# Kernel optimization log

Hardware: AMD Instinct MI355X
Metric: run time of the kernel (lower is better)

Reference implementation:

```python
import jax, jax.numpy as jnp
import numpy as np

N_QUBITS = 14
N_LAYERS = 4
N_CLASSES = 10
BATCH = 1024


def apply_1q(state, gate, wire):
    """Apply a 2x2 gate ([2,2] shared or [B,2,2] batched) to `wire` of state [B,2,...,2]."""
    s = jnp.moveaxis(state, wire + 1, -1)
    shp = s.shape
    s = s.reshape(shp[0], -1, 2)
    if gate.ndim == 3:
        s = jnp.einsum('bij,bkj->bki', gate, s)
    else:
        s = jnp.einsum('ij,bkj->bki', gate, s)
    return jnp.moveaxis(s.reshape(shp), -1, wire + 1)


def apply_cnot(state, c, t):
    s = jnp.moveaxis(state, (c + 1, t + 1), (-2, -1))
    s = jnp.stack([s[..., 0, :], s[..., 1, ::-1]], axis=-2)
    return jnp.moveaxis(s, (-2, -1), (c + 1, t + 1))


def simulate(x, q_params):
    """Batched statevector sim of: RY(x_i) embed -> BasicEntanglerLayers(RX + CNOT ring) -> <Z_i>."""
    B, n = x.shape
    state = jnp.zeros((B,) + (2,) * n, jnp.complex64)
    state = state.at[(slice(None),) + (0,) * n].set(1.0)

    # RY(x_i) on each wire (angles batched per sample)
    c, s = jnp.cos(0.5 * x), jnp.sin(0.5 * x)
    for w in range(n):
        g = jnp.stack([jnp.stack([c[:, w], -s[:, w]], -1),
                       jnp.stack([s[:, w], c[:, w]], -1)], -2).astype(jnp.complex64)  # [B,2,2]
        state = apply_1q(state, g, w)

    # BasicEntanglerLayers: per layer RX(weights[l,i]) on every wire, then CNOT ring
    cw, sw = jnp.cos(0.5 * q_params), jnp.sin(0.5 * q_params)
    n_layers = q_params.shape[0]
    for l in range(n_layers):
        for w in range(n):
            cc = cw[l, w].astype(jnp.complex64)
            isw = (-1j) * sw[l, w].astype(jnp.complex64)
            g = jnp.stack([jnp.stack([cc, isw]), jnp.stack([isw, cc])])  # [2,2] RX
            state = apply_1q(state, g, w)
        if n == 2:
            state = apply_cnot(state, 0, 1)
        else:
            for w in range(n):
                state = apply_cnot(state, w, (w + 1) % n)

    # <Z_i> = P(bit_i=0) - P(bit_i=1)
    p = jnp.abs(state) ** 2  # [B,2,...,2] real
    axes_all = tuple(range(1, n + 1))
    z = []
    for w in range(n):
        pw = jnp.sum(p, axis=tuple(a for a in axes_all if a != w + 1))  # [B,2]
        z.append(pw[:, 0] - pw[:, 1])
    return jnp.stack(z, -1).astype(jnp.float32)  # [B, n]


def setup_inputs() -> dict:
    key = jax.random.key(0)
    k1, k2, k3, k4 = jax.random.split(key, 4)
    x = jax.random.normal(k1, (BATCH, N_QUBITS), dtype=jnp.float32)
    q_params = 0.01 * jax.random.normal(k2, (N_LAYERS, N_QUBITS), dtype=jnp.float32)
    fc_w = jax.random.normal(k3, (N_CLASSES, N_QUBITS), dtype=jnp.float32) / np.sqrt(N_QUBITS)
    fc_b = jax.random.normal(k4, (N_CLASSES,), dtype=jnp.float32) * 0.01
    return {"x": x, "q_params": q_params, "fc_w": fc_w, "fc_b": fc_b}


def reference(x, q_params, fc_w, fc_b):
    q_out = simulate(x, q_params)            # [B, n_qubits]
    logits = q_out @ fc_w.T + fc_b           # [B, n_classes]
    return logits
```

## Files before the change

kernel.cpp:

```cpp
#include <hip/hip_runtime.h>
#include <hip/hip_fp16.h>
#include <math.h>


#define NQ 14
#define NSTATE (1 << NQ)
#define NLAYERS 4
#define NCLASSES 10
#define BLOCK 512
#define PADN (NSTATE + (NSTATE >> 5))

template<int LO, int M, int STEP, bool IS_RX, bool INIT, int PRE_CTRL, int POST_CTRL, bool CHAIN, bool FINAL>
__device__ __forceinline__ void run_pass(__half2* __restrict__ st,
                                         const __half2* __restrict__ cw,
                                         const __half2* __restrict__ sw,
                                         float* __restrict__ zloc)
{
  constexpr int KN  = 1 << M;
  constexpr int NCH = NSTATE >> M;
  __half2 c[M], s[M];
#pragma unroll
  for (int j = 0; j < M; ++j) { c[j] = cw[j]; s[j] = sw[j]; }

  for (int chunk = threadIdx.x; chunk < NCH; chunk += BLOCK) {
    const int low   = chunk & ((1 << LO) - 1);
    const int high  = chunk >> LO;
    const int base  = low | (high << (LO + M));
    const int pbase = base + (base >> 5);
    __half2 a[KN];
    if constexpr (INIT) {
#pragma unroll
      for (int k = 0; k < KN; ++k) a[k] = __floats2half2_rn(0.f, 0.f);
      if (chunk == 0) a[0] = __floats2half2_rn(1.f, 0.f);
    } else {
#pragma unroll
      for (int k = 0; k < KN; ++k) a[k] = st[pbase + k * STEP];
    }
    if constexpr (PRE_CTRL >= 0) {
      if ((base >> PRE_CTRL) & 1) {
#pragma unroll
        for (int k = 0; k < KN; k += 2) { __half2 t = a[k]; a[k] = a[k + 1]; a[k + 1] = t; }
      }
    }
#pragma unroll
    for (int j = 0; j < M; ++j) {
#pragma unroll
      for (int k = 0; k < KN; ++k) {
        if ((k & (1 << j)) == 0) {
          const int k1 = k | (1 << j);
          const __half2 a0 = a[k], a1 = a[k1];
          if constexpr (IS_RX) {
            a[k]  = __hfma2(s[j], __lowhigh2highlow(a1), __hmul2(c[j], a0));
            a[k1] = __hfma2(s[j], __lowhigh2highlow(a0), __hmul2(c[j], a1));
          } else {
            a[k]  = __hsub2(__hmul2(c[j], a0), __hmul2(s[j], a1));
            a[k1] = __hfma2(s[j], a0, __hmul2(c[j], a1));
          }
        }
      }
    }
    if constexpr (POST_CTRL >= 0) {
      if ((base >> POST_CTRL) & 1) {
#pragma unroll
        for (int k = 0; k < KN; k += 2) { __half2 t = a[k]; a[k] = a[k + 1]; a[k + 1] = t; }
      }
    }
    if constexpr (CHAIN) {
#pragma unroll
      for (int j = 0; j < M - 1; ++j) {
#pragma unroll
        for (int k = 0; k < KN; ++k) {
          if ((k & (1 << j)) != 0 && (k & (1 << (j + 1))) == 0) {
            const int k2 = k | (1 << (j + 1));
            __half2 t = a[k]; a[k] = a[k2]; a[k2] = t;
          }
        }
      }
    }
    if constexpr (FINAL) {
      float ssum = 0.f, sb0 = 0.f, sb1 = 0.f, sb2 = 0.f, sb3 = 0.f;
#pragma unroll
      for (int k = 0; k < KN; ++k) {
        const float2 v = __half22float2(a[k]);
        const float p = fmaf(v.x, v.x, v.y * v.y);
        ssum += p;
        if (k & 1) sb0 += p;
        if (k & 2) sb1 += p;
        if (k & 4) sb2 += p;
        if (k & 8) sb3 += p;
      }
      zloc[10] += ssum - 2.f * sb0;
      zloc[11] += ssum - 2.f * sb1;
      zloc[12] += ssum - 2.f * sb2;
      zloc[13] += ssum - 2.f * sb3;
      const float z0 = ssum - 2.f * sb3;
      zloc[0] += (base & 1) ? -z0 : z0;
#pragma unroll
      for (int w = 1; w < 10; ++w) zloc[w] += ((base >> w) & 1) ? -ssum : ssum;
    } else {
#pragma unroll
      for (int k = 0; k < KN; ++k) st[pbase + k * STEP] = a[k];
    }
  }
}

__global__ __launch_bounds__(BLOCK) void qsim_kernel(
    const float* __restrict__ x, const float* __restrict__ qp,
    const float* __restrict__ fcw, const float* __restrict__ fcb,
    float* __restrict__ out)
{
  extern __shared__ unsigned char smem[];
  __half2* st  = (__half2*)smem;
  __half2* ryc = st + PADN;
  __half2* rys = ryc + NQ;
  __half2* rxc = rys + NQ;
  __half2* rxs = rxc + NLAYERS * NQ;
  float*   zbuf  = (float*)(rxs + NLAYERS * NQ);
  float*   zpart = zbuf + NQ;

  const int b   = blockIdx.x;
  const int tid = threadIdx.x;

  if (tid < NQ) {
    float sv, cv;
    sincosf(0.5f * x[b * NQ + tid], &sv, &cv);
    ryc[tid] = __floats2half2_rn(cv, cv);
    rys[tid] = __floats2half2_rn(sv, sv);
  } else if (tid >= 64 && tid < 64 + NLAYERS * NQ) {
    const int k = tid - 64;
    float sv, cv;
    sincosf(0.5f * qp[k], &sv, &cv);
    rxc[k] = __floats2half2_rn(cv, cv);
    rxs[k] = __floats2half2_rn(sv, -sv);
  }
  __syncthreads();

  run_pass<0, 5, 1,    false, true,  -1, -1, false, false>(st, ryc,      rys,      nullptr); __syncthreads();
  run_pass<5, 5, 33,   false, false, -1, -1, false, false>(st, ryc + 5,  rys + 5,  nullptr); __syncthreads();
  run_pass<10, 4, 1056,false, false, -1, -1, false, false>(st, ryc + 10, rys + 10, nullptr); __syncthreads();

  float zloc[NQ];
#pragma unroll
  for (int w = 0; w < NQ; ++w) zloc[w] = 0.f;

#pragma unroll
  for (int l = 0; l < NLAYERS; ++l) {
    const __half2* lc = rxc + l * NQ;
    const __half2* ls = rxs + l * NQ;
    if (l == 0) run_pass<0, 5, 1, true, false, -1, -1, true, false>(st, lc, ls, nullptr);
    else        run_pass<0, 5, 1, true, false, 13, -1, true, false>(st, lc, ls, nullptr);
    __syncthreads();
    run_pass<5, 5, 33, true, false, -1, 4, true, false>(st, lc + 5, ls + 5, nullptr);
    __syncthreads();
    if (l < NLAYERS - 1) {
      run_pass<10, 4, 1056, true, false, -1, 9, true, false>(st, lc + 10, ls + 10, nullptr);
      __syncthreads();
    } else {
      run_pass<10, 4, 1056, true, false, -1, 9, true, true>(st, lc + 10, ls + 10, zloc);
    }
  }

#pragma unroll
  for (int w = 0; w < NQ; ++w) {
#pragma unroll
    for (int off = 32; off > 0; off >>= 1)
      zloc[w] += __shfl_down(zloc[w], off, 64);
  }
  const int wave = tid >> 6, lane = tid & 63;
  if (lane == 0) {
#pragma unroll
    for (int w = 0; w < NQ; ++w) zpart[wave * NQ + w] = zloc[w];
  }
  __syncthreads();
  if (tid < NQ) {
    float acc = 0.f;
#pragma unroll
    for (int v = 0; v < BLOCK / 64; ++v) acc += zpart[v * NQ + tid];
    zbuf[tid] = acc;
  }
  __syncthreads();

  if (tid < NCLASSES) {
    float acc = fcb[tid];
#pragma unroll
    for (int w = 0; w < NQ; ++w) acc = fmaf(zbuf[w], fcw[tid * NQ + w], acc);
    out[b * NCLASSES + tid] = acc;
  }
}

extern "C" void kernel_launch(void* const* d_in, const int* in_sizes, int n_in,
                              void* d_out, int out_size, void* d_ws, size_t ws_size,
                              hipStream_t stream) {
  const float* x   = (const float*)d_in[0];
  const float* qp  = (const float*)d_in[1];
  const float* fcw = (const float*)d_in[2];
  const float* fcb = (const float*)d_in[3];
  float* out = (float*)d_out;
  const int B = in_sizes[0] / NQ;

  const size_t shmem = (size_t)PADN * sizeof(__half2)
                     + (size_t)(2 * NQ + 2 * NLAYERS * NQ) * sizeof(__half2)
                     + (size_t)(NQ + (BLOCK / 64) * NQ) * sizeof(float);
  (void)hipFuncSetAttribute((const void*)qsim_kernel,
                            hipFuncAttributeMaxDynamicSharedMemorySize, (int)shmem);
  qsim_kernel<<<B, BLOCK, shmem, stream>>>(x, qp, fcw, fcb, out);
}
```

Measured before the change: 145.2 us.

## Rewrite statevector sim as MFMA matrix products with fused RX+CNOT unitaries

Replaces the per-thread half2 butterfly passes with 32x32 and 16x16 complex unitaries, built per layer from RX angles with the CNOT permutations folded in, and applied via f16 MFMA instructions on split real/imaginary planes in LDS with XOR swizzling. The RY embedding plus the first RX block is computed analytically as a product state instead of through passes. This aims to move the gate arithmetic onto matrix cores and cut the number of passes. In exchange it adds per-pass matrix construction, extra barriers, and a larger LDS footprint (about 67KB) that limits blocks per CU.

Measured after the change: 146.1 us. No clear change (+0.6%).

```diff
diff --git a/kernel.cpp b/kernel.cpp
--- a/kernel.cpp
+++ b/kernel.cpp
@@ -4,162 +4,303 @@
 
 
 #define NQ 14
-#define NSTATE (1 << NQ)
 #define NLAYERS 4
 #define NCLASSES 10
 #define BLOCK 512
-#define PADN (NSTATE + (NSTATE >> 5))
-
-template<int LO, int M, int STEP, bool IS_RX, bool INIT, int PRE_CTRL, int POST_CTRL, bool CHAIN, bool FINAL>
-__device__ __forceinline__ void run_pass(__half2* __restrict__ st,
-                                         const __half2* __restrict__ cw,
-                                         const __half2* __restrict__ sw,
-                                         float* __restrict__ zloc)
-{
-  constexpr int KN  = 1 << M;
-  constexpr int NCH = NSTATE >> M;
-  __half2 c[M], s[M];
-#pragma unroll
-  for (int j = 0; j < M; ++j) { c[j] = cw[j]; s[j] = sw[j]; }
-
-  for (int chunk = threadIdx.x; chunk < NCH; chunk += BLOCK) {
-    const int low   = chunk & ((1 << LO) - 1);
-    const int high  = chunk >> LO;
-    const int base  = low | (high << (LO + M));
-    const int pbase = base + (base >> 5);
-    __half2 a[KN];
-    if constexpr (INIT) {
-#pragma unroll
-      for (int k = 0; k < KN; ++k) a[k] = __floats2half2_rn(0.f, 0.f);
-      if (chunk == 0) a[0] = __floats2half2_rn(1.f, 0.f);
+
+typedef _Float16 f16;
+typedef _Float16 f16x8 __attribute__((ext_vector_type(8)));
+typedef _Float16 f16x4 __attribute__((ext_vector_type(4)));
+typedef float f32x4 __attribute__((ext_vector_type(4)));
+typedef unsigned int u32;
+typedef u32 u32x4 __attribute__((ext_vector_type(4)));
+
+__device__ __forceinline__ f32x4 mf(f16x8 a, f16x8 b, f32x4 c) {
+  return __builtin_amdgcn_mfma_f32_16x16x32_f16(a, b, c, 0, 0, 0);
+}
+
+__device__ __forceinline__ int finv5(int n) {
+  n ^= ((n >> 3) & 1) << 4;
+  n ^= ((n >> 2) & 1) << 3;
+  n ^= ((n >> 1) & 1) << 2;
+  n ^= (n & 1) << 1;
+  return n;
+}
+__device__ __forceinline__ int finv3(int n) {
+  n ^= ((n >> 2) & 1) << 3;
+  n ^= ((n >> 1) & 1) << 2;
+  n ^= (n & 1) << 1;
+  return n;
+}
+
+__device__ __forceinline__ void splitB(f16x8 b, int s, f16x8& br, f16x8& bi) {
+  u32x4 u = __builtin_bit_cast(u32x4, b);
+  const u32 m0 = s ? 0xFFFF0000u : 0x0000FFFFu;
+  const u32 m1 = s ? 0x0000FFFFu : 0xFFFF0000u;
+  u32x4 r;
+  r[0] = u[0] & m0; r[1] = u[1] & m1; r[2] = u[2] & m1; r[3] = u[3] & m0;
+  u32x4 ii;
+  ii[0] = u[0] ^ r[0]; ii[1] = u[1] ^ r[1]; ii[2] = u[2] ^ r[2]; ii[3] = u[3] ^ r[3];
+  br = __builtin_bit_cast(f16x8, r);
+  bi = __builtin_bit_cast(f16x8, ii);
+}
+
+__device__ __forceinline__ void build32(f16* Bc, const float* qc, const float* qs,
+                                        int base, int tid) {
+  const float c0 = qc[base], c1 = qc[base+1], c2 = qc[base+2], c3 = qc[base+3], c4 = qc[base+4];
+  const float s0 = qs[base], s1 = qs[base+1], s2 = qs[base+2], s3 = qs[base+3], s4 = qs[base+4];
+#pragma unroll
+  for (int e = tid; e < 1024; e += BLOCK) {
+    const int n = e >> 5, k = e & 31;
+    const int d = finv5(n) ^ k;
+    float mag = ((d & 1) ? s0 : c0) * ((d & 2) ? s1 : c1);
+    mag *= ((d & 4) ? s2 : c2) * ((d & 8) ? s3 : c3);
+    mag *= ((d & 16) ? s4 : c4);
+    const int t = __popc(d) & 3;
+    Bc[n * 32 + k] = (f16)((t == 1 || t == 2) ? -mag : mag);
+  }
+}
+
+__device__ __forceinline__ void buildC(f16* Bc, const float* qc, const float* qs,
+                                       int base, int tid) {
+  const float c0 = qc[base], c1 = qc[base+1], c2 = qc[base+2], c3 = qc[base+3];
+  const float s0 = qs[base], s1 = qs[base+1], s2 = qs[base+2], s3 = qs[base+3];
+  if (tid < 512) {
+    const int n = tid >> 5, k = tid & 31;
+    float v = 0.f;
+    if (k < 16) {
+      const int d = finv3(n) ^ k;
+      float mag = ((d & 1) ? s0 : c0) * ((d & 2) ? s1 : c1);
+      mag *= ((d & 4) ? s2 : c2) * ((d & 8) ? s3 : c3);
+      const int t = __popc(d) & 3;
+      v = (t == 1 || t == 2) ? -mag : mag;
+    }
+    Bc[n * 32 + k] = (f16)v;
+  }
+}
+
+template<bool CTRL>
+__device__ __forceinline__ void pass32(f16* __restrict__ reP, f16* __restrict__ imP,
+                                       const f16* __restrict__ Bc, int tid) {
+  const int lane = tid & 63, wave = tid >> 6;
+  const int q = lane >> 4, cc = lane & 15;
+  int n0 = cc, n1 = cc | 16;
+  if (CTRL && wave >= 4) { n0 ^= 31; n1 ^= 31; }
+  const int pq = (0x6 >> q) & 1;
+  f16x8 br0, bi0, br1, bi1;
+  {
+    const f16x8 b0 = *(const f16x8*)(Bc + n0 * 32 + 8 * q);
+    const f16x8 b1 = *(const f16x8*)(Bc + n1 * 32 + 8 * q);
+    splitB(b0, ((n0 >> 4) ^ pq) & 1, br0, bi0);
+    splitB(b1, ((n1 >> 4) ^ pq) & 1, br1, bi1);
+  }
+  f16x4 outR[8], outI[8];
+#pragma unroll
+  for (int i = 0; i < 4; ++i) {
+    const int mt = wave * 4 + i;
+    const int pA = ((mt * 16 + cc) * 32 + 8 * q) ^ ((mt & 7) << 3);
+    const f16x8 Ar = *(const f16x8*)(reP + pA);
+    const f16x8 Ai = *(const f16x8*)(imP + pA);
+    const f16x8 nAi = -Ai;
+#pragma unroll
+    for (int nt = 0; nt < 2; ++nt) {
+      const f16x8 br = nt ? br1 : br0;
+      const f16x8 bi = nt ? bi1 : bi0;
+      f32x4 aR = {0.f, 0.f, 0.f, 0.f}, aI = {0.f, 0.f, 0.f, 0.f};
+      aR = mf(Ar, br, aR); aR = mf(nAi, bi, aR);
+      aI = mf(Ar, bi, aI); aI = mf(Ai, br, aI);
+      outR[i * 2 + nt] = __builtin_convertvector(aR, f16x4);
+      outI[i * 2 + nt] = __builtin_convertvector(aI, f16x4);
+    }
+  }
+  __syncthreads();
+#pragma unroll
+  for (int i = 0; i < 4; ++i) {
+#pragma unroll
+    for (int nt = 0; nt < 2; ++nt) {
+      const int n5 = nt * 16 + cc;
+      const int rr = (wave * 4 + i) * 16 + 4 * q;
+      const int pS = (rr | (n5 << 9)) ^ ((n5 & 7) << 3);
+      *(f16x4*)(reP + pS) = outR[i * 2 + nt];
+      *(f16x4*)(imP + pS) = outI[i * 2 + nt];
+    }
+  }
+}
+
+template<bool FINAL>
+__device__ __forceinline__ void passC(f16* __restrict__ reP, f16* __restrict__ imP,
+                                      const f16* __restrict__ Bc, int tid,
+                                      float* __restrict__ zloc) {
+  const int lane = tid & 63, wave = tid >> 6;
+  const int q = lane >> 4, cc = lane & 15;
+  int n0 = cc;
+  if (wave >= 4) n0 ^= 15;
+  const int pq = (0x6 >> q) & 1;
+  f16x8 br, bi;
+  {
+    const f16x8 b = *(const f16x8*)(Bc + n0 * 32 + 8 * q);
+    splitB(b, ((n0 >> 3) ^ pq) & 1, br, bi);
+  }
+  f16x4 outR[8], outI[8];
+#pragma unroll
+  for (int i = 0; i < 8; ++i) {
+    const int mt = wave * 8 + i;
+    const int pA = ((mt * 16 + cc) * 16 + 8 * (q & 1)) ^ (((mt >> 1) & 7) << 3);
+    const f16x8 Ar = *(const f16x8*)(reP + pA);
+    const f16x8 Ai = *(const f16x8*)(imP + pA);
+    const f16x8 nAi = -Ai;
+    f32x4 aR = {0.f, 0.f, 0.f, 0.f}, aI = {0.f, 0.f, 0.f, 0.f};
+    aR = mf(Ar, br, aR); aR = mf(nAi, bi, aR);
+    aI = mf(Ar, bi, aI); aI = mf(Ai, br, aI);
+    if constexpr (FINAL) {
+      float p0 = aR[0]*aR[0] + aI[0]*aI[0];
+      float p1 = aR[1]*aR[1] + aI[1]*aI[1];
+      float p2 = aR[2]*aR[2] + aI[2]*aI[2];
+      float p3 = aR[3]*aR[3] + aI[3]*aI[3];
+      if (cc & 8) { float t = p0; p0 = p1; p1 = t; t = p2; p2 = p3; p3 = t; }
+      const float ps = p0 + p1 + p2 + p3;
+      zloc[0] += (p0 - p1) + (p2 - p3);
+      zloc[1] += (p0 + p1) - (p2 + p3);
+      zloc[2] += (q & 1) ? -ps : ps;
+      zloc[3] += (q & 2) ? -ps : ps;
+#pragma unroll
+      for (int w = 0; w < 6; ++w) zloc[4 + w] += ((mt >> w) & 1) ? -ps : ps;
+#pragma unroll
+      for (int w = 0; w < 4; ++w) zloc[10 + w] += ((cc >> w) & 1) ? -ps : ps;
     } else {
-#pragma unroll
-      for (int k = 0; k < KN; ++k) a[k] = st[pbase + k * STEP];
-    }
-    if constexpr (PRE_CTRL >= 0) {
-      if ((base >> PRE_CTRL) & 1) {
-#pragma unroll
-        for (int k = 0; k < KN; k += 2) { __half2 t = a[k]; a[k] = a[k + 1]; a[k + 1] = t; }
+      if (cc & 8) {
+        f32x4 tR = aR, tI = aI;
+        aR[0] = tR[1]; aR[1] = tR[0]; aR[2] = tR[3]; aR[3] = tR[2];
+        aI[0] = tI[1]; aI[1] = tI[0]; aI[2] = tI[3]; aI[3] = tI[2];
       }
-    }
-#pragma unroll
-    for (int j = 0; j < M; ++j) {
-#pragma unroll
-      for (int k = 0; k < KN; ++k) {
-        if ((k & (1 << j)) == 0) {
-          const int k1 = k | (1 << j);
-          const __half2 a0 = a[k], a1 = a[k1];
-          if constexpr (IS_RX) {
-            a[k]  = __hfma2(s[j], __lowhigh2highlow(a1), __hmul2(c[j], a0));
-            a[k1] = __hfma2(s[j], __lowhigh2highlow(a0), __hmul2(c[j], a1));
-          } else {
-            a[k]  = __hsub2(__hmul2(c[j], a0), __hmul2(s[j], a1));
-            a[k1] = __hfma2(s[j], a0, __hmul2(c[j], a1));
-          }
-        }
-      }
-    }
-    if constexpr (POST_CTRL >= 0) {
-      if ((base >> POST_CTRL) & 1) {
-#pragma unroll
-        for (int k = 0; k < KN; k += 2) { __half2 t = a[k]; a[k] = a[k + 1]; a[k + 1] = t; }
-      }
-    }
-    if constexpr (CHAIN) {
-#pragma unroll
-      for (int j = 0; j < M - 1; ++j) {
-#pragma unroll
-        for (int k = 0; k < KN; ++k) {
-          if ((k & (1 << j)) != 0 && (k & (1 << (j + 1))) == 0) {
-            const int k2 = k | (1 << (j + 1));
-            __half2 t = a[k]; a[k] = a[k2]; a[k2] = t;
-          }
-        }
-      }
-    }
-    if constexpr (FINAL) {
-      float ssum = 0.f, sb0 = 0.f, sb1 = 0.f, sb2 = 0.f, sb3 = 0.f;
-#pragma unroll
-      for (int k = 0; k < KN; ++k) {
-        const float2 v = __half22float2(a[k]);
-        const float p = fmaf(v.x, v.x, v.y * v.y);
-        ssum += p;
-        if (k & 1) sb0 += p;
-        if (k & 2) sb1 += p;
-        if (k & 4) sb2 += p;
-        if (k & 8) sb3 += p;
-      }
-      zloc[10] += ssum - 2.f * sb0;
-      zloc[11] += ssum - 2.f * sb1;
-      zloc[12] += ssum - 2.f * sb2;
-      zloc[13] += ssum - 2.f * sb3;
-      const float z0 = ssum - 2.f * sb3;
-      zloc[0] += (base & 1) ? -z0 : z0;
-#pragma unroll
-      for (int w = 1; w < 10; ++w) zloc[w] += ((base >> w) & 1) ? -ssum : ssum;
-    } else {
-#pragma unroll
-      for (int k = 0; k < KN; ++k) st[pbase + k * STEP] = a[k];
-    }
-  }
-}
-
-__global__ __launch_bounds__(BLOCK) void qsim_kernel(
+      outR[i] = __builtin_convertvector(aR, f16x4);
+      outI[i] = __builtin_convertvector(aI, f16x4);
+    }
+  }
+  if constexpr (!FINAL) {
+    __syncthreads();
+#pragma unroll
+    for (int i = 0; i < 8; ++i) {
+      const int rr = (wave * 8 + i) * 16 + 4 * q;
+      const int nI = rr | (cc << 10);
+      const int pS = nI ^ ((((rr >> 9) | ((cc & 3) << 1)) & 7) << 3);
+      *(f16x4*)(reP + pS) = outR[i];
+      *(f16x4*)(imP + pS) = outI[i];
+    }
+  }
+}
+
+__global__ __launch_bounds__(BLOCK, 4) void qsim_kernel(
     const float* __restrict__ x, const float* __restrict__ qp,
     const float* __restrict__ fcw, const float* __restrict__ fcb,
-    float* __restrict__ out)
-{
+    float* __restrict__ out) {
   extern __shared__ unsigned char smem[];
-  __half2* st  = (__half2*)smem;
-  __half2* ryc = st + PADN;
-  __half2* rys = ryc + NQ;
-  __half2* rxc = rys + NQ;
-  __half2* rxs = rxc + NLAYERS * NQ;
-  float*   zbuf  = (float*)(rxs + NLAYERS * NQ);
-  float*   zpart = zbuf + NQ;
-
-  const int b   = blockIdx.x;
+  f16* reP = (f16*)smem;
+  f16* imP = reP + 16384;
+  unsigned char* scr = (unsigned char*)(imP + 16384);
+  f16* Bc = (f16*)scr;
+  float* qc = (float*)(scr + 2048);
+  float* qs = qc + 56;
+  float* xc = qs + 56;
+  float* xs = xc + 14;
+
+  const int b = blockIdx.x;
   const int tid = threadIdx.x;
 
   if (tid < NQ) {
-    float sv, cv;
-    sincosf(0.5f * x[b * NQ + tid], &sv, &cv);
-    ryc[tid] = __floats2half2_rn(cv, cv);
-    rys[tid] = __floats2half2_rn(sv, sv);
+    float sv, cv; sincosf(0.5f * x[b * NQ + tid], &sv, &cv);
+    xc[tid] = cv; xs[tid] = sv;
   } else if (tid >= 64 && tid < 64 + NLAYERS * NQ) {
     const int k = tid - 64;
-    float sv, cv;
-    sincosf(0.5f * qp[k], &sv, &cv);
-    rxc[k] = __floats2half2_rn(cv, cv);
-    rxs[k] = __floats2half2_rn(sv, -sv);
-  }
-  __syncthreads();
-
-  run_pass<0, 5, 1,    false, true,  -1, -1, false, false>(st, ryc,      rys,      nullptr); __syncthreads();
-  run_pass<5, 5, 33,   false, false, -1, -1, false, false>(st, ryc + 5,  rys + 5,  nullptr); __syncthreads();
-  run_pass<10, 4, 1056,false, false, -1, -1, false, false>(st, ryc + 10, rys + 10, nullptr); __syncthreads();
+    float sv, cv; sincosf(0.5f * qp[k], &sv, &cv);
+    qc[k] = cv; qs[k] = sv;
+  }
+  __syncthreads();
+
+  float* Flo  = (float*)scr;
+  float* psi  = Flo + 32;
+  float* PsiR = psi + 32;
+  float* PsiI = PsiR + 32;
+  if (tid < 32) {
+    float f = 1.f;
+#pragma unroll
+    for (int j = 0; j < 5; ++j) f *= ((tid >> j) & 1) ? xs[5 + j] : xc[5 + j];
+    Flo[tid] = f;
+  } else if (tid < 64) {
+    const int k = tid - 32;
+    float f = 1.f;
+#pragma unroll
+    for (int j = 0; j < 5; ++j) f *= ((k >> j) & 1) ? xs[j] : xc[j];
+    psi[k] = f;
+  }
+  __syncthreads();
+  if (tid < 32) {
+    const float c0 = qc[0], c1 = qc[1], c2 = qc[2], c3 = qc[3], c4 = qc[4];
+    const float s0 = qs[0], s1 = qs[1], s2 = qs[2], s3 = qs[3], s4 = qs[4];
+    const int a = finv5(tid);
+    float ar = 0.f, ai = 0.f;
+    for (int k = 0; k < 32; ++k) {
+      const int d = a ^ k;
+      float mag = ((d & 1) ? s0 : c0) * ((d & 2) ? s1 : c1);
+      mag *= ((d & 4) ? s2 : c2) * ((d & 8) ? s3 : c3);
+      mag *= ((d & 16) ? s4 : c4);
+      mag *= psi[k];
+      const int t = __popc(d) & 3;
+      if (t == 0) ar += mag; else if (t == 1) ai -= mag;
+      else if (t == 2) ar -= mag; else ai += mag;
+    }
+    PsiR[tid] = ar; PsiI[tid] = ai;
+  }
+  __syncthreads();
+  {
+    float fhi = 1.f;
+#pragma unroll
+    for (int j = 0; j < 4; ++j) fhi *= ((tid >> j) & 1) ? xs[10 + j] : xc[10 + j];
+    const float cr = fhi * PsiR[tid >> 4], ci = fhi * PsiI[tid >> 4];
+    const int pconst = ((tid >> 4) & 7) << 3;
+#pragma unroll
+    for (int kb = 0; kb < 4; ++kb) {
+      f16x8 hr, hi;
+#pragma unroll
+      for (int j = 0; j < 8; ++j) {
+        const float F = Flo[8 * kb + j];
+        hr[j] = (f16)(F * cr);
+        hi[j] = (f16)(F * ci);
+      }
+      const int pb = (tid * 32 + 8 * kb) ^ pconst;
+      *(f16x8*)(reP + pb) = hr;
+      *(f16x8*)(imP + pb) = hi;
+    }
+  }
+  __syncthreads();
+
+  build32(Bc, qc, qs, 0 * NQ + 5, tid);  __syncthreads();
+  pass32<true>(reP, imP, Bc, tid);       __syncthreads();
+  buildC(Bc, qc, qs, 0 * NQ + 10, tid);  __syncthreads();
+  passC<false>(reP, imP, Bc, tid, nullptr); __syncthreads();
+#pragma unroll
+  for (int l = 1; l < 3; ++l) {
+    build32(Bc, qc, qs, l * NQ + 0, tid);  __syncthreads();
+    pass32<false>(reP, imP, Bc, tid);      __syncthreads();
+    build32(Bc, qc, qs, l * NQ + 5, tid);  __syncthreads();
+    pass32<true>(reP, imP, Bc, tid);       __syncthreads();
+    buildC(Bc, qc, qs, l * NQ + 10, tid);  __syncthreads();
+    passC<false>(reP, imP, Bc, tid, nullptr); __syncthreads();
+  }
+  build32(Bc, qc, qs, 3 * NQ + 0, tid);  __syncthreads();
+  pass32<false>(reP, imP, Bc, tid);      __syncthreads();
+  build32(Bc, qc, qs, 3 * NQ + 5, tid);  __syncthreads();
+  pass32<true>(reP, imP, Bc, tid);       __syncthreads();
+  buildC(Bc, qc, qs, 3 * NQ + 10, tid);  __syncthreads();
 
   float zloc[NQ];
 #pragma unroll
   for (int w = 0; w < NQ; ++w) zloc[w] = 0.f;
-
-#pragma unroll
-  for (int l = 0; l < NLAYERS; ++l) {
-    const __half2* lc = rxc + l * NQ;
-    const __half2* ls = rxs + l * NQ;
-    if (l == 0) run_pass<0, 5, 1, true, false, -1, -1, true, false>(st, lc, ls, nullptr);
-    else        run_pass<0, 5, 1, true, false, 13, -1, true, false>(st, lc, ls, nullptr);
-    __syncthreads();
-    run_pass<5, 5, 33, true, false, -1, 4, true, false>(st, lc + 5, ls + 5, nullptr);
-    __syncthreads();
-    if (l < NLAYERS - 1) {
-      run_pass<10, 4, 1056, true, false, -1, 9, true, false>(st, lc + 10, ls + 10, nullptr);
-      __syncthreads();
-    } else {
-      run_pass<10, 4, 1056, true, false, -1, 9, true, true>(st, lc + 10, ls + 10, zloc);
-    }
-  }
-
+  passC<true>(reP, imP, Bc, tid, zloc);
+  __syncthreads();
+
+  float* zpart = (float*)scr;
+  float* zbuf  = zpart + 112;
 #pragma unroll
   for (int w = 0; w < NQ; ++w) {
 #pragma unroll
@@ -173,13 +314,12 @@
   }
   __syncthreads();
   if (tid < NQ) {
-    float acc = 0.f;
-#pragma unroll
-    for (int v = 0; v < BLOCK / 64; ++v) acc += zpart[v * NQ + tid];
-    zbuf[tid] = acc;
-  }
-  __syncthreads();
-
+    float a = 0.f;
+#pragma unroll
+    for (int v = 0; v < 8; ++v) a += zpart[v * NQ + tid];
+    zbuf[tid] = a;
+  }
+  __syncthreads();
   if (tid < NCLASSES) {
     float acc = fcb[tid];
 #pragma unroll
@@ -198,9 +338,7 @@
   float* out = (float*)d_out;
   const int B = in_sizes[0] / NQ;
 
-  const size_t shmem = (size_t)PADN * sizeof(__half2)
-                     + (size_t)(2 * NQ + 2 * NLAYERS * NQ) * sizeof(__half2)
-                     + (size_t)(NQ + (BLOCK / 64) * NQ) * sizeof(float);
+  const size_t shmem = 65536 + 2048 + 448 + 112;
   (void)hipFuncSetAttribute((const void*)qsim_kernel,
                             hipFuncAttributeMaxDynamicSharedMemorySize, (int)shmem);
   qsim_kernel<<<B, BLOCK, shmem, stream>>>(x, qp, fcw, fcb, out);
```
